# Optimization experiments

Hardware: AMD Instinct MI355X
Metric: run time of the kernel (lower is better)

The kernel has to match this reference:

```python
import jax, jax.numpy as jnp
import numpy as np

NEG_SLOPE = 0.2


def gat_layer(x, W, a_src, a_dst, b, src, dst, num_nodes, heads, out_c, concat):
    # Linear transform per head: [N, heads, out_c]
    h = (x @ W).reshape(num_nodes, heads, out_c)
    # Per-node attention logits for source/dest roles: [N, heads]
    e_src = jnp.einsum('nhc,hc->nh', h, a_src)
    e_dst = jnp.einsum('nhc,hc->nh', h, a_dst)
    # Edge-wise scores (gather), LeakyReLU: [E, heads]
    e = jax.nn.leaky_relu(e_src[src] + e_dst[dst], negative_slope=NEG_SLOPE)
    # Segment softmax over incoming edges of each destination node
    m = jax.ops.segment_max(e, dst, num_segments=num_nodes)
    ex = jnp.exp(e - m[dst])
    denom = jax.ops.segment_sum(ex, dst, num_segments=num_nodes)
    alpha = ex / denom[dst]                       # [E, heads]
    # Weighted scatter-aggregate of source messages: [N, heads, out_c]
    out = jax.ops.segment_sum(h[src] * alpha[:, :, None], dst, num_segments=num_nodes)
    if concat:
        out = out.reshape(num_nodes, heads * out_c)
    else:
        out = out.mean(axis=1)
    return out + b


def setup_inputs() -> dict:
    key = jax.random.key(0)
    ks = jax.random.split(key, 12)
    N, E = 50000, 800000
    in_c, out_c, heads = 128, 32, 4
    x = jax.random.normal(ks[0], (N, in_c), dtype=jnp.float32)
    edge_index = jax.random.randint(ks[1], (2, E), 0, N, dtype=jnp.int64)
    s1 = 1.0 / np.sqrt(in_c)
    W1 = jax.random.normal(ks[2], (in_c, heads * out_c), dtype=jnp.float32) * s1
    a_src1 = jax.random.normal(ks[3], (heads, out_c), dtype=jnp.float32) * 0.1
    a_dst1 = jax.random.normal(ks[4], (heads, out_c), dtype=jnp.float32) * 0.1
    b1 = jnp.zeros((heads * out_c,), dtype=jnp.float32)
    s2 = 1.0 / np.sqrt(heads * out_c)
    W2 = jax.random.normal(ks[5], (heads * out_c, out_c), dtype=jnp.float32) * s2
    a_src2 = jax.random.normal(ks[6], (1, out_c), dtype=jnp.float32) * 0.1
    a_dst2 = jax.random.normal(ks[7], (1, out_c), dtype=jnp.float32) * 0.1
    b2 = jnp.zeros((out_c,), dtype=jnp.float32)
    return {"x": x, "edge_index": edge_index, "W1": W1, "a_src1": a_src1,
            "a_dst1": a_dst1, "b1": b1, "W2": W2, "a_src2": a_src2,
            "a_dst2": a_dst2, "b2": b2}


def reference(x, edge_index, W1, a_src1, a_dst1, b1, W2, a_src2, a_dst2, b2):
    N = x.shape[0]
    heads, out_c = a_src1.shape
    # add_self_loops=True (PyG default)
    loops = jnp.arange(N, dtype=edge_index.dtype)
    src = jnp.concatenate([edge_index[0], loops])
    dst = jnp.concatenate([edge_index[1], loops])
    h1 = gat_layer(x, W1, a_src1, a_dst1, b1, src, dst, N, heads, out_c, concat=True)
    h1 = jax.nn.elu(h1)
    out = gat_layer(h1, W2, a_src2, a_dst2, b2, src, dst, N, 1, out_c, concat=False)
    return out
```

## Files before the change

kernel.cpp:

```cpp
#include <hip/hip_runtime.h>
#include <hip/hip_bf16.h>

#define LRELU_SLOPE 0.2f
#define NB_SHIFT 7

typedef __attribute__((ext_vector_type(8))) short short8;
typedef __attribute__((ext_vector_type(4))) float float4v;

__device__ inline float b2f(unsigned short u) {
    union { unsigned int i; float f; } v; v.i = ((unsigned int)u) << 16; return v.f;
}
__device__ inline unsigned short f2b(float f) {
    union { float f; unsigned int i; } v; v.f = f;
    unsigned int x = v.i;
    unsigned int r = x + 0x7fffu + ((x >> 16) & 1u);
    return (unsigned short)(r >> 16);
}
__device__ inline float lrelu(float x) { return x > 0.f ? x : LRELU_SLOPE * x; }

__global__ __launch_bounds__(256) void hist_kernel(const int* __restrict__ dst,
                                                   int E, int Etot, int nb, int nblk,
                                                   int chunk, int* __restrict__ cnt) {
    __shared__ int hist[512];
    int blk = blockIdx.x;
    for (int i = threadIdx.x; i < nb; i += 256) hist[i] = 0;
    __syncthreads();
    int lo = blk * chunk;
    int hi = lo + chunk; if (hi > Etot) hi = Etot;
    for (int i = lo + threadIdx.x; i < hi; i += 256) {
        int d = (i < E) ? dst[i] : (i - E);
        atomicAdd(&hist[d >> NB_SHIFT], 1);
    }
    __syncthreads();
    for (int b = threadIdx.x; b < nb; b += 256)
        cnt[b * nblk + blk] = hist[b];
}

__global__ __launch_bounds__(1024) void scanA_kernel(int* cnt, int* bsum, int M) {
    __shared__ int tile[1024];
    int i = blockIdx.x * 1024 + threadIdx.x;
    int v = (i < M) ? cnt[i] : 0;
    tile[threadIdx.x] = v;
    __syncthreads();
    for (int off = 1; off < 1024; off <<= 1) {
        int t = (threadIdx.x >= (unsigned)off) ? tile[threadIdx.x - off] : 0;
        __syncthreads();
        tile[threadIdx.x] += t;
        __syncthreads();
    }
    int incl = tile[threadIdx.x];
    if (i < M) cnt[i] = incl - v;
    if (threadIdx.x == 1023) bsum[blockIdx.x] = incl;
}

__global__ __launch_bounds__(256) void scanB_kernel(int* __restrict__ bsum, int nb) {
    __shared__ int tile[256];
    int v = (threadIdx.x < (unsigned)nb) ? bsum[threadIdx.x] : 0;
    tile[threadIdx.x] = v;
    __syncthreads();
    for (int off = 1; off < 256; off <<= 1) {
        int t = (threadIdx.x >= (unsigned)off) ? tile[threadIdx.x - off] : 0;
        __syncthreads();
        tile[threadIdx.x] += t;
        __syncthreads();
    }
    if (threadIdx.x < (unsigned)nb) bsum[threadIdx.x] = tile[threadIdx.x] - v;
}

__global__ __launch_bounds__(256) void partition_kernel(
        const int* __restrict__ src, const int* __restrict__ dst,
        int E, int Etot, int nb, int nblk, int chunk,
        const int* __restrict__ cnt, const int* __restrict__ boff,
        int2* __restrict__ bkt) {
    __shared__ int cur[512];
    int blk = blockIdx.x;
    for (int b = threadIdx.x; b < nb; b += 256) {
        int idx = b * nblk + blk;
        cur[b] = cnt[idx] + boff[idx >> 10];
    }
    __syncthreads();
    int lo = blk * chunk;
    int hi = lo + chunk; if (hi > Etot) hi = Etot;
    for (int i = lo + threadIdx.x; i < hi; i += 256) {
        int s, d;
        if (i < E) { s = src[i]; d = dst[i]; }
        else       { s = d = i - E; }
        int pos = atomicAdd(&cur[d >> NB_SHIFT], 1);
        bkt[pos] = make_int2(s, d);
    }
}

__global__ __launch_bounds__(256) void finalize_kernel(
        const int2* __restrict__ bkt, const int* __restrict__ cnt,
        const int* __restrict__ boff, int nb, int nblk,
        const float* __restrict__ es, const float* __restrict__ ed,
        int* __restrict__ ptr, int2* __restrict__ csr, float* __restrict__ w1,
        int N, int Etot) {
    __shared__ int deg[128];
    __shared__ int scn[128];
    __shared__ int cur[128];
    int b = blockIdx.x;
    int idx0 = b * nblk;
    int base = cnt[idx0] + boff[idx0 >> 10];
    int nextbase;
    if (b + 1 < nb) {
        int idx1 = (b + 1) * nblk;
        nextbase = cnt[idx1] + boff[idx1 >> 10];
    } else nextbase = Etot;
    int count = nextbase - base;
    int node0 = b << NB_SHIFT;
    int nodes = N - node0; if (nodes > 128) nodes = 128;

    if (threadIdx.x < 128) deg[threadIdx.x] = 0;
    __syncthreads();
    for (int i = threadIdx.x; i < count; i += 256)
        atomicAdd(&deg[bkt[base + i].y - node0], 1);
    __syncthreads();
    int v = (threadIdx.x < 128) ? deg[threadIdx.x] : 0;
    if (threadIdx.x < 128) scn[threadIdx.x] = v;
    __syncthreads();
    for (int off = 1; off < 128; off <<= 1) {
        int t = (threadIdx.x < 128 && threadIdx.x >= (unsigned)off) ? scn[threadIdx.x - off] : 0;
        __syncthreads();
        if (threadIdx.x < 128) scn[threadIdx.x] += t;
        __syncthreads();
    }
    if (threadIdx.x < 128) {
        int excl = scn[threadIdx.x] - v;
        cur[threadIdx.x] = excl;
        if (threadIdx.x < nodes) ptr[node0 + threadIdx.x] = base + excl;
    }
    if (b == nb - 1 && threadIdx.x == 0) ptr[N] = Etot;
    __syncthreads();
    for (int i = threadIdx.x; i < count; i += 256) {
        int2 sd = bkt[base + i];
        int pos = base + atomicAdd(&cur[sd.y - node0], 1);
        csr[pos] = sd;
        float4 a = *(const float4*)&es[sd.x * 4];
        float4 bb = *(const float4*)&ed[sd.y * 4];
        float4 ww;
        ww.x = __expf(lrelu(a.x + bb.x));
        ww.y = __expf(lrelu(a.y + bb.y));
        ww.z = __expf(lrelu(a.z + bb.z));
        ww.w = __expf(lrelu(a.w + bb.w));
        *(float4*)&w1[(size_t)pos * 4] = ww;
    }
}

__global__ __launch_bounds__(256) void gemm1_mfma_kernel(
        const float* __restrict__ x, const float* __restrict__ W1,
        unsigned short* __restrict__ h1b, int N) {
    __shared__ unsigned short xs[64][136];
    __shared__ unsigned short wt[128][136];
    int tid = threadIdx.x;
    int n0 = blockIdx.x * 64;

    for (int i = tid; i < 128 * 128; i += 256) {
        int k = i >> 7, n = i & 127;
        wt[n][k] = f2b(W1[i]);
    }
    for (int i = tid; i < 64 * 128; i += 256) {
        int r = i >> 7, k = i & 127;
        int row = n0 + r; if (row >= N) row = N - 1;
        xs[r][k] = f2b(x[(size_t)row * 128 + k]);
    }
    __syncthreads();

    int wave = tid >> 6;
    int lane = tid & 63;
    int lrow = lane & 15;
    int quad = lane >> 4;

    short8 afr[4];
#pragma unroll
    for (int kc = 0; kc < 4; kc++)
        afr[kc] = *(const short8*)&xs[wave * 16 + lrow][kc * 32 + quad * 8];

#pragma unroll
    for (int ct = 0; ct < 8; ct++) {
        float4v acc = {0.f, 0.f, 0.f, 0.f};
#pragma unroll
        for (int kc = 0; kc < 4; kc++) {
            short8 bfr = *(const short8*)&wt[ct * 16 + lrow][kc * 32 + quad * 8];
            acc = __builtin_amdgcn_mfma_f32_16x16x32_bf16(afr[kc], bfr, acc, 0, 0, 0);
        }
#pragma unroll
        for (int r = 0; r < 4; r++) {
            int grow = n0 + wave * 16 + quad * 4 + r;
            if (grow < N)
                h1b[grow * 128 + ct * 16 + lrow] = f2b(acc[r]);
        }
    }
}

__global__ __launch_bounds__(256) void gemm2_mfma_kernel(
        const unsigned short* __restrict__ h1e, const float* __restrict__ W2,
        unsigned short* __restrict__ h2b, int N) {
    __shared__ unsigned short xs[64][136];
    __shared__ unsigned short wt[32][136];
    int tid = threadIdx.x;
    int n0 = blockIdx.x * 64;

    for (int i = tid; i < 128 * 32; i += 256) {
        int k = i >> 5, n = i & 31;
        wt[n][k] = f2b(W2[i]);
    }
    {
        const unsigned int* srcp = (const unsigned int*)(h1e + (size_t)n0 * 128);
        int rows = (N - n0) < 64 ? (N - n0) : 64;
        int maxu = rows * 64;
        for (int i = tid; i < 4096; i += 256) {
            unsigned int v = (i < maxu) ? srcp[i] : 0u;
            int r = i >> 6, cp = (i & 63) << 1;
            *(unsigned int*)&xs[r][cp] = v;
        }
    }
    __syncthreads();

    int wave = tid >> 6;
    int lane = tid & 63;
    int lrow = lane & 15;
    int quad = lane >> 4;

    short8 afr[4];
#pragma unroll
    for (int kc = 0; kc < 4; kc++)
        afr[kc] = *(const short8*)&xs[wave * 16 + lrow][kc * 32 + quad * 8];

#pragma unroll
    for (int ct = 0; ct < 2; ct++) {
        float4v acc = {0.f, 0.f, 0.f, 0.f};
#pragma unroll
        for (int kc = 0; kc < 4; kc++) {
            short8 bfr = *(const short8*)&wt[ct * 16 + lrow][kc * 32 + quad * 8];
            acc = __builtin_amdgcn_mfma_f32_16x16x32_bf16(afr[kc], bfr, acc, 0, 0, 0);
        }
#pragma unroll
        for (int r = 0; r < 4; r++) {
            int grow = n0 + wave * 16 + quad * 4 + r;
            if (grow < N)
                h2b[(size_t)grow * 32 + ct * 16 + lrow] = f2b(acc[r]);
        }
    }
}

__global__ void dots1_kernel(const unsigned short* __restrict__ h1b,
                             const float* __restrict__ a_src,
                             const float* __restrict__ a_dst,
                             float* __restrict__ es, float* __restrict__ ed,
                             int N4) {
    int t = blockIdx.x * 256 + threadIdx.x;
    if (t >= N4) return;
    int h = t & 3;
    const unsigned int* hp = (const unsigned int*)(h1b + (size_t)t * 32);
    const float* ap = a_src + h * 32;
    const float* bp = a_dst + h * 32;
    float s = 0.f, d = 0.f;
#pragma unroll
    for (int j = 0; j < 16; j++) {
        unsigned int u = hp[j];
        float v0 = b2f((unsigned short)(u & 0xffffu));
        float v1 = b2f((unsigned short)(u >> 16));
        s += v0 * ap[2 * j] + v1 * ap[2 * j + 1];
        d += v0 * bp[2 * j] + v1 * bp[2 * j + 1];
    }
    es[t] = s; ed[t] = d;
}

__global__ void dots2_kernel(const unsigned short* __restrict__ h2b,
                             const float* __restrict__ a_src,
                             const float* __restrict__ a_dst,
                             float* __restrict__ es, float* __restrict__ ed,
                             int N) {
    int t = blockIdx.x * 256 + threadIdx.x;
    if (t >= N) return;
    const unsigned int* hp = (const unsigned int*)(h2b + (size_t)t * 32);
    const float* ap = a_src;
    const float* bp = a_dst;
    float s = 0.f, d = 0.f;
#pragma unroll
    for (int j = 0; j < 16; j++) {
        unsigned int u = hp[j];
        float v0 = b2f((unsigned short)(u & 0xffffu));
        float v1 = b2f((unsigned short)(u >> 16));
        s += v0 * ap[2 * j] + v1 * ap[2 * j + 1];
        d += v0 * bp[2 * j] + v1 * bp[2 * j + 1];
    }
    es[t] = s; ed[t] = d;
}

__global__ void weights2_kernel(const int2* __restrict__ csr,
                                const float* __restrict__ es,
                                const float* __restrict__ ed,
                                float* __restrict__ w2, int Etot) {
    int e = blockIdx.x * 256 + threadIdx.x;
    if (e >= Etot) return;
    int2 sd = csr[e];
    w2[e] = __expf(lrelu(es[sd.x] + ed[sd.y]));
}

__global__ __launch_bounds__(256) void agg1_kernel(
        const unsigned int* __restrict__ h1u, const float* __restrict__ w1,
        const int2* __restrict__ csr, const int* __restrict__ ptr,
        const float* __restrict__ b1, unsigned int* __restrict__ h1e_u, int N) {
    int wave = threadIdx.x >> 6;
    int lane = threadIdx.x & 63;
    int n = blockIdx.x * 4 + wave;
    if (n >= N) return;
    int h = lane >> 4;
    int start = ptr[n], end = ptr[n + 1];
    float acc0 = 0.f, acc1 = 0.f, wsum = 0.f;
    int i = start;
    for (; i + 4 <= end; i += 4) {
        int s0 = csr[i + 0].x;
        int s1 = csr[i + 1].x;
        int s2 = csr[i + 2].x;
        int s3 = csr[i + 3].x;
        float v0 = w1[(size_t)(i + 0) * 4 + h];
        float v1 = w1[(size_t)(i + 1) * 4 + h];
        float v2 = w1[(size_t)(i + 2) * 4 + h];
        float v3 = w1[(size_t)(i + 3) * 4 + h];
        unsigned int g0 = h1u[(s0 << 6) + lane];
        unsigned int g1 = h1u[(s1 << 6) + lane];
        unsigned int g2 = h1u[(s2 << 6) + lane];
        unsigned int g3 = h1u[(s3 << 6) + lane];
        acc0 += v0 * b2f((unsigned short)(g0 & 0xffffu))
              + v1 * b2f((unsigned short)(g1 & 0xffffu))
              + v2 * b2f((unsigned short)(g2 & 0xffffu))
              + v3 * b2f((unsigned short)(g3 & 0xffffu));
        acc1 += v0 * b2f((unsigned short)(g0 >> 16))
              + v1 * b2f((unsigned short)(g1 >> 16))
              + v2 * b2f((unsigned short)(g2 >> 16))
              + v3 * b2f((unsigned short)(g3 >> 16));
        wsum += (v0 + v1) + (v2 + v3);
    }
    for (; i < end; i++) {
        int s = csr[i].x;
        float v = w1[(size_t)i * 4 + h];
        unsigned int g = h1u[(s << 6) + lane];
        acc0 += v * b2f((unsigned short)(g & 0xffffu));
        acc1 += v * b2f((unsigned short)(g >> 16));
        wsum += v;
    }
    float r = 1.f / wsum;
    float2 bb = ((const float2*)b1)[lane];
    float o0 = acc0 * r + bb.x;
    float o1 = acc1 * r + bb.y;
    o0 = o0 > 0.f ? o0 : __expf(o0) - 1.f;
    o1 = o1 > 0.f ? o1 : __expf(o1) - 1.f;
    h1e_u[(n << 6) + lane] = (unsigned int)f2b(o0) | ((unsigned int)f2b(o1) << 16);
}

__global__ __launch_bounds__(256) void agg2_kernel(
        const unsigned int* __restrict__ h2u, const float* __restrict__ w2,
        const int2* __restrict__ csr, const int* __restrict__ ptr,
        const float* __restrict__ b2, float* __restrict__ out, int N) {
    int lane = threadIdx.x & 63;
    int g = lane >> 4;
    int n = blockIdx.x * 16 + (threadIdx.x >> 6) * 4 + g;
    if (n >= N) return;
    int cl = lane & 15;
    int start = ptr[n], end = ptr[n + 1];
    float acc0 = 0.f, acc1 = 0.f, wsum = 0.f;
    int i = start;
    for (; i + 4 <= end; i += 4) {
        int s0 = csr[i + 0].x;
        int s1 = csr[i + 1].x;
        int s2 = csr[i + 2].x;
        int s3 = csr[i + 3].x;
        float v0 = w2[i + 0];
        float v1 = w2[i + 1];
        float v2 = w2[i + 2];
        float v3 = w2[i + 3];
        unsigned int g0 = h2u[(s0 << 4) + cl];
        unsigned int g1 = h2u[(s1 << 4) + cl];
        unsigned int g2 = h2u[(s2 << 4) + cl];
        unsigned int g3 = h2u[(s3 << 4) + cl];
        acc0 += v0 * b2f((unsigned short)(g0 & 0xffffu))
              + v1 * b2f((unsigned short)(g1 & 0xffffu))
              + v2 * b2f((unsigned short)(g2 & 0xffffu))
              + v3 * b2f((unsigned short)(g3 & 0xffffu));
        acc1 += v0 * b2f((unsigned short)(g0 >> 16))
              + v1 * b2f((unsigned short)(g1 >> 16))
              + v2 * b2f((unsigned short)(g2 >> 16))
              + v3 * b2f((unsigned short)(g3 >> 16));
        wsum += (v0 + v1) + (v2 + v3);
    }
    for (; i < end; i++) {
        int s = csr[i].x;
        float v = w2[i];
        unsigned int gg = h2u[(s << 4) + cl];
        acc0 += v * b2f((unsigned short)(gg & 0xffffu));
        acc1 += v * b2f((unsigned short)(gg >> 16));
        wsum += v;
    }
    float r = 1.f / wsum;
    float2 bb = ((const float2*)b2)[cl];
    float2 o;
    o.x = acc0 * r + bb.x;
    o.y = acc1 * r + bb.y;
    ((float2*)out)[(size_t)n * 16 + cl] = o;
}

extern "C" void kernel_launch(void* const* d_in, const int* in_sizes, int n_in,
                              void* d_out, int out_size, void* d_ws, size_t ws_size,
                              hipStream_t stream) {
    const float* x      = (const float*)d_in[0];
    const int*   ei     = (const int*)  d_in[1];
    const float* W1     = (const float*)d_in[2];
    const float* a_src1 = (const float*)d_in[3];
    const float* a_dst1 = (const float*)d_in[4];
    const float* b1     = (const float*)d_in[5];
    const float* W2     = (const float*)d_in[6];
    const float* a_src2 = (const float*)d_in[7];
    const float* a_dst2 = (const float*)d_in[8];
    const float* b2     = (const float*)d_in[9];
    float* outp = (float*)d_out;

    const int N = in_sizes[0] / 128;
    const int E = in_sizes[1] / 2;
    const int Etot = E + N;

    const int* src = ei;
    const int* dst = ei + E;

    const int nb   = (N + 127) >> 7;
    const int nblk = 128;
    const int chunk = (Etot + nblk - 1) / nblk;
    const int M = nb * nblk;
    const int nbA = (M + 1023) / 1024;

    char* w = (char*)d_ws;
    unsigned short* h1b = (unsigned short*)(w + 0);
    unsigned short* h1e = (unsigned short*)(w + 12800000);
    unsigned short* h2b = (unsigned short*)(w + 25600000);
    float* es1  = (float*)(w + 28800000);
    float* ed1  = (float*)(w + 29600000);
    float* es2  = (float*)(w + 30400000);
    float* ed2  = (float*)(w + 30600000);
    int*   ptr  = (int*)  (w + 30800000);
    int*   bsum = (int*)  (w + 31000064);
    int*   cnt  = (int*)  (w + 31001088);
    int2*  csr  = (int2*) (w + 31201280);
    int2*  bkt  = (int2*) (w + 38001280);
    float* w1   = (float*)(w + 44801280);
    float* w2   = (float*)(w + 58401280);

    gemm1_mfma_kernel<<<(N + 63) / 64, 256, 0, stream>>>(x, W1, h1b, N);
    dots1_kernel<<<(N * 4 + 255) / 256, 256, 0, stream>>>(h1b, a_src1, a_dst1, es1, ed1, N * 4);

    hist_kernel<<<nblk, 256, 0, stream>>>(dst, E, Etot, nb, nblk, chunk, cnt);
    scanA_kernel<<<nbA, 1024, 0, stream>>>(cnt, bsum, M);
    scanB_kernel<<<1, 256, 0, stream>>>(bsum, nbA);
    partition_kernel<<<nblk, 256, 0, stream>>>(src, dst, E, Etot, nb, nblk, chunk,
                                               cnt, bsum, bkt);
    finalize_kernel<<<nb, 256, 0, stream>>>(bkt, cnt, bsum, nb, nblk, es1, ed1,
                                            ptr, csr, w1, N, Etot);

    agg1_kernel<<<(N + 3) / 4, 256, 0, stream>>>((const unsigned int*)h1b, w1, csr, ptr,
                                                 b1, (unsigned int*)h1e, N);

    gemm2_mfma_kernel<<<(N + 63) / 64, 256, 0, stream>>>(h1e, W2, h2b, N);
    dots2_kernel<<<(N + 255) / 256, 256, 0, stream>>>(h2b, a_src2, a_dst2, es2, ed2, N);
    weights2_kernel<<<(Etot + 255) / 256, 256, 0, stream>>>(csr, es2, ed2, w2, Etot);
    agg2_kernel<<<(N + 15) / 16, 256, 0, stream>>>((const unsigned int*)h2b, w2, csr, ptr,
                                                   b2, outp, N);
}
```

Baseline: 229.8 us.

## Fuse attention dots into GEMMs, compute layer-2 weights inline, shrink CSR

The per-node attention dot products move into the epilogues of both MFMA GEMM kernels, which stage the bf16 output tile in shared memory; this removes the dots1 and dots2 launches and their reread of h. The layer-2 edge weights are now computed on the fly inside agg2, which drops the weights2 kernel and the w2 buffer. The CSR now stores only source indices (int instead of int2), cutting its write and read traffic. agg1 is unrolled to 8 edges per step to keep more gathers in flight. In exchange, agg2 recomputes exp per edge and the GEMMs gain extra barriers and epilogue work.

```diff
diff --git a/kernel.cpp b/kernel.cpp
--- a/kernel.cpp
+++ b/kernel.cpp
@@ -94,7 +94,7 @@
         const int2* __restrict__ bkt, const int* __restrict__ cnt,
         const int* __restrict__ boff, int nb, int nblk,
         const float* __restrict__ es, const float* __restrict__ ed,
-        int* __restrict__ ptr, int2* __restrict__ csr, float* __restrict__ w1,
+        int* __restrict__ ptr, int* __restrict__ csr_src, float* __restrict__ w1,
         int N, int Etot) {
     __shared__ int deg[128];
     __shared__ int scn[128];
@@ -135,7 +135,7 @@
     for (int i = threadIdx.x; i < count; i += 256) {
         int2 sd = bkt[base + i];
         int pos = base + atomicAdd(&cur[sd.y - node0], 1);
-        csr[pos] = sd;
+        csr_src[pos] = sd.x;
         float4 a = *(const float4*)&es[sd.x * 4];
         float4 bb = *(const float4*)&ed[sd.y * 4];
         float4 ww;
@@ -149,7 +149,9 @@
 
 __global__ __launch_bounds__(256) void gemm1_mfma_kernel(
         const float* __restrict__ x, const float* __restrict__ W1,
-        unsigned short* __restrict__ h1b, int N) {
+        const float* __restrict__ a_src, const float* __restrict__ a_dst,
+        unsigned short* __restrict__ h1b, float* __restrict__ es,
+        float* __restrict__ ed, int N) {
     __shared__ unsigned short xs[64][136];
     __shared__ unsigned short wt[128][136];
     int tid = threadIdx.x;
@@ -175,6 +177,7 @@
 #pragma unroll
     for (int kc = 0; kc < 4; kc++)
         afr[kc] = *(const short8*)&xs[wave * 16 + lrow][kc * 32 + quad * 8];
+    __syncthreads();
 
 #pragma unroll
     for (int ct = 0; ct < 8; ct++) {
@@ -186,16 +189,42 @@
         }
 #pragma unroll
         for (int r = 0; r < 4; r++) {
-            int grow = n0 + wave * 16 + quad * 4 + r;
+            int lr = wave * 16 + quad * 4 + r;
+            int grow = n0 + lr;
+            unsigned short hb = f2b(acc[r]);
+            xs[lr][ct * 16 + lrow] = hb;
             if (grow < N)
-                h1b[grow * 128 + ct * 16 + lrow] = f2b(acc[r]);
-        }
+                h1b[grow * 128 + ct * 16 + lrow] = hb;
+        }
+    }
+    __syncthreads();
+
+    int row = tid >> 2, h = tid & 3;
+    int rg = n0 + row;
+    if (rg < N) {
+        const float* ap = a_src + h * 32;
+        const float* bp = a_dst + h * 32;
+        float s = 0.f, d = 0.f;
+#pragma unroll
+        for (int c2 = 0; c2 < 16; c2++) {
+            unsigned int u = *(const unsigned int*)&xs[row][h * 32 + 2 * c2];
+            float v0 = b2f((unsigned short)(u & 0xffffu));
+            float v1 = b2f((unsigned short)(u >> 16));
+            float2 a = *(const float2*)&ap[2 * c2];
+            float2 b = *(const float2*)&bp[2 * c2];
+            s += v0 * a.x + v1 * a.y;
+            d += v0 * b.x + v1 * b.y;
+        }
+        es[rg * 4 + h] = s;
+        ed[rg * 4 + h] = d;
     }
 }
 
 __global__ __launch_bounds__(256) void gemm2_mfma_kernel(
         const unsigned short* __restrict__ h1e, const float* __restrict__ W2,
-        unsigned short* __restrict__ h2b, int N) {
+        const float* __restrict__ a_src, const float* __restrict__ a_dst,
+        unsigned short* __restrict__ h2b, float* __restrict__ es,
+        float* __restrict__ ed, int N) {
     __shared__ unsigned short xs[64][136];
     __shared__ unsigned short wt[32][136];
     int tid = threadIdx.x;
@@ -226,6 +255,7 @@
 #pragma unroll
     for (int kc = 0; kc < 4; kc++)
         afr[kc] = *(const short8*)&xs[wave * 16 + lrow][kc * 32 + quad * 8];
+    __syncthreads();
 
 #pragma unroll
     for (int ct = 0; ct < 2; ct++) {
@@ -237,71 +267,39 @@
         }
 #pragma unroll
         for (int r = 0; r < 4; r++) {
-            int grow = n0 + wave * 16 + quad * 4 + r;
+            int lr = wave * 16 + quad * 4 + r;
+            int grow = n0 + lr;
+            unsigned short hb = f2b(acc[r]);
+            xs[lr][ct * 16 + lrow] = hb;
             if (grow < N)
-                h2b[(size_t)grow * 32 + ct * 16 + lrow] = f2b(acc[r]);
-        }
-    }
-}
-
-__global__ void dots1_kernel(const unsigned short* __restrict__ h1b,
-                             const float* __restrict__ a_src,
-                             const float* __restrict__ a_dst,
-                             float* __restrict__ es, float* __restrict__ ed,
-                             int N4) {
-    int t = blockIdx.x * 256 + threadIdx.x;
-    if (t >= N4) return;
-    int h = t & 3;
-    const unsigned int* hp = (const unsigned int*)(h1b + (size_t)t * 32);
-    const float* ap = a_src + h * 32;
-    const float* bp = a_dst + h * 32;
-    float s = 0.f, d = 0.f;
-#pragma unroll
-    for (int j = 0; j < 16; j++) {
-        unsigned int u = hp[j];
-        float v0 = b2f((unsigned short)(u & 0xffffu));
-        float v1 = b2f((unsigned short)(u >> 16));
-        s += v0 * ap[2 * j] + v1 * ap[2 * j + 1];
-        d += v0 * bp[2 * j] + v1 * bp[2 * j + 1];
-    }
-    es[t] = s; ed[t] = d;
-}
-
-__global__ void dots2_kernel(const unsigned short* __restrict__ h2b,
-                             const float* __restrict__ a_src,
-                             const float* __restrict__ a_dst,
-                             float* __restrict__ es, float* __restrict__ ed,
-                             int N) {
-    int t = blockIdx.x * 256 + threadIdx.x;
-    if (t >= N) return;
-    const unsigned int* hp = (const unsigned int*)(h2b + (size_t)t * 32);
-    const float* ap = a_src;
-    const float* bp = a_dst;
-    float s = 0.f, d = 0.f;
-#pragma unroll
-    for (int j = 0; j < 16; j++) {
-        unsigned int u = hp[j];
-        float v0 = b2f((unsigned short)(u & 0xffffu));
-        float v1 = b2f((unsigned short)(u >> 16));
-        s += v0 * ap[2 * j] + v1 * ap[2 * j + 1];
-        d += v0 * bp[2 * j] + v1 * bp[2 * j + 1];
-    }
-    es[t] = s; ed[t] = d;
-}
-
-__global__ void weights2_kernel(const int2* __restrict__ csr,
-                                const float* __restrict__ es,
-                                const float* __restrict__ ed,
-                                float* __restrict__ w2, int Etot) {
-    int e = blockIdx.x * 256 + threadIdx.x;
-    if (e >= Etot) return;
-    int2 sd = csr[e];
-    w2[e] = __expf(lrelu(es[sd.x] + ed[sd.y]));
+                h2b[(size_t)grow * 32 + ct * 16 + lrow] = hb;
+        }
+    }
+    __syncthreads();
+
+    if (tid < 64) {
+        int rg = n0 + tid;
+        if (rg < N) {
+            float s = 0.f, d = 0.f;
+#pragma unroll
+            for (int c2 = 0; c2 < 16; c2++) {
+                unsigned int u = *(const unsigned int*)&xs[tid][2 * c2];
+                float v0 = b2f((unsigned short)(u & 0xffffu));
+                float v1 = b2f((unsigned short)(u >> 16));
+                float2 a = *(const float2*)&a_src[2 * c2];
+                float2 b = *(const float2*)&a_dst[2 * c2];
+                s += v0 * a.x + v1 * a.y;
+                d += v0 * b.x + v1 * b.y;
+            }
+            es[rg] = s;
+            ed[rg] = d;
+        }
+    }
 }
 
 __global__ __launch_bounds__(256) void agg1_kernel(
         const unsigned int* __restrict__ h1u, const float* __restrict__ w1,
-        const int2* __restrict__ csr, const int* __restrict__ ptr,
+        const int* __restrict__ csr, const int* __restrict__ ptr,
         const float* __restrict__ b1, unsigned int* __restrict__ h1e_u, int N) {
     int wave = threadIdx.x >> 6;
     int lane = threadIdx.x & 63;
@@ -311,31 +309,38 @@
     int start = ptr[n], end = ptr[n + 1];
     float acc0 = 0.f, acc1 = 0.f, wsum = 0.f;
     int i = start;
+    for (; i + 8 <= end; i += 8) {
+        int s[8]; float v[8]; unsigned int g[8];
+#pragma unroll
+        for (int k = 0; k < 8; k++) s[k] = csr[i + k];
+#pragma unroll
+        for (int k = 0; k < 8; k++) v[k] = w1[(size_t)(i + k) * 4 + h];
+#pragma unroll
+        for (int k = 0; k < 8; k++) g[k] = h1u[(s[k] << 6) + lane];
+#pragma unroll
+        for (int k = 0; k < 8; k++) {
+            acc0 += v[k] * b2f((unsigned short)(g[k] & 0xffffu));
+            acc1 += v[k] * b2f((unsigned short)(g[k] >> 16));
+            wsum += v[k];
+        }
+    }
     for (; i + 4 <= end; i += 4) {
-        int s0 = csr[i + 0].x;
-        int s1 = csr[i + 1].x;
-        int s2 = csr[i + 2].x;
-        int s3 = csr[i + 3].x;
-        float v0 = w1[(size_t)(i + 0) * 4 + h];
-        float v1 = w1[(size_t)(i + 1) * 4 + h];
-        float v2 = w1[(size_t)(i + 2) * 4 + h];
-        float v3 = w1[(size_t)(i + 3) * 4 + h];
-        unsigned int g0 = h1u[(s0 << 6) + lane];
-        unsigned int g1 = h1u[(s1 << 6) + lane];
-        unsigned int g2 = h1u[(s2 << 6) + lane];
-        unsigned int g3 = h1u[(s3 << 6) + lane];
-        acc0 += v0 * b2f((unsigned short)(g0 & 0xffffu))
-              + v1 * b2f((unsigned short)(g1 & 0xffffu))
-              + v2 * b2f((unsigned short)(g2 & 0xffffu))
-              + v3 * b2f((unsigned short)(g3 & 0xffffu));
-        acc1 += v0 * b2f((unsigned short)(g0 >> 16))
-              + v1 * b2f((unsigned short)(g1 >> 16))
-              + v2 * b2f((unsigned short)(g2 >> 16))
-              + v3 * b2f((unsigned short)(g3 >> 16));
-        wsum += (v0 + v1) + (v2 + v3);
+        int s[4]; float v[4]; unsigned int g[4];
+#pragma unroll
+        for (int k = 0; k < 4; k++) s[k] = csr[i + k];
+#pragma unroll
+        for (int k = 0; k < 4; k++) v[k] = w1[(size_t)(i + k) * 4 + h];
+#pragma unroll
+        for (int k = 0; k < 4; k++) g[k] = h1u[(s[k] << 6) + lane];
+#pragma unroll
+        for (int k = 0; k < 4; k++) {
+            acc0 += v[k] * b2f((unsigned short)(g[k] & 0xffffu));
+            acc1 += v[k] * b2f((unsigned short)(g[k] >> 16));
+            wsum += v[k];
+        }
     }
     for (; i < end; i++) {
-        int s = csr[i].x;
+        int s = csr[i];
         float v = w1[(size_t)i * 4 + h];
         unsigned int g = h1u[(s << 6) + lane];
         acc0 += v * b2f((unsigned short)(g & 0xffffu));
@@ -352,46 +357,40 @@
 }
 
 __global__ __launch_bounds__(256) void agg2_kernel(
-        const unsigned int* __restrict__ h2u, const float* __restrict__ w2,
-        const int2* __restrict__ csr, const int* __restrict__ ptr,
-        const float* __restrict__ b2, float* __restrict__ out, int N) {
+        const unsigned int* __restrict__ h2u, const float* __restrict__ es,
+        const float* __restrict__ ed, const int* __restrict__ csr,
+        const int* __restrict__ ptr, const float* __restrict__ b2,
+        float* __restrict__ out, int N) {
     int lane = threadIdx.x & 63;
-    int g = lane >> 4;
-    int n = blockIdx.x * 16 + (threadIdx.x >> 6) * 4 + g;
+    int n = blockIdx.x * 16 + (threadIdx.x >> 6) * 4 + (lane >> 4);
     if (n >= N) return;
     int cl = lane & 15;
+    float edl = ed[n];
     int start = ptr[n], end = ptr[n + 1];
     float acc0 = 0.f, acc1 = 0.f, wsum = 0.f;
     int i = start;
     for (; i + 4 <= end; i += 4) {
-        int s0 = csr[i + 0].x;
-        int s1 = csr[i + 1].x;
-        int s2 = csr[i + 2].x;
-        int s3 = csr[i + 3].x;
-        float v0 = w2[i + 0];
-        float v1 = w2[i + 1];
-        float v2 = w2[i + 2];
-        float v3 = w2[i + 3];
-        unsigned int g0 = h2u[(s0 << 4) + cl];
-        unsigned int g1 = h2u[(s1 << 4) + cl];
-        unsigned int g2 = h2u[(s2 << 4) + cl];
-        unsigned int g3 = h2u[(s3 << 4) + cl];
-        acc0 += v0 * b2f((unsigned short)(g0 & 0xffffu))
-              + v1 * b2f((unsigned short)(g1 & 0xffffu))
-              + v2 * b2f((unsigned short)(g2 & 0xffffu))
-              + v3 * b2f((unsigned short)(g3 & 0xffffu));
-        acc1 += v0 * b2f((unsigned short)(g0 >> 16))
-              + v1 * b2f((unsigned short)(g1 >> 16))
-              + v2 * b2f((unsigned short)(g2 >> 16))
-              + v3 * b2f((unsigned short)(g3 >> 16));
-        wsum += (v0 + v1) + (v2 + v3);
+        int s[4]; float e[4]; unsigned int g[4];
+#pragma unroll
+        for (int k = 0; k < 4; k++) s[k] = csr[i + k];
+#pragma unroll
+        for (int k = 0; k < 4; k++) e[k] = es[s[k]];
+#pragma unroll
+        for (int k = 0; k < 4; k++) g[k] = h2u[(s[k] << 4) + cl];
+#pragma unroll
+        for (int k = 0; k < 4; k++) {
+            float v = __expf(lrelu(e[k] + edl));
+            acc0 += v * b2f((unsigned short)(g[k] & 0xffffu));
+            acc1 += v * b2f((unsigned short)(g[k] >> 16));
+            wsum += v;
+        }
     }
     for (; i < end; i++) {
-        int s = csr[i].x;
-        float v = w2[i];
-        unsigned int gg = h2u[(s << 4) + cl];
-        acc0 += v * b2f((unsigned short)(gg & 0xffffu));
-        acc1 += v * b2f((unsigned short)(gg >> 16));
+        int s = csr[i];
+        float v = __expf(lrelu(es[s] + edl));
+        unsigned int g = h2u[(s << 4) + cl];
+        acc0 += v * b2f((unsigned short)(g & 0xffffu));
+        acc1 += v * b2f((unsigned short)(g >> 16));
         wsum += v;
     }
     float r = 1.f / wsum;
@@ -441,13 +440,12 @@
     int*   ptr  = (int*)  (w + 30800000);
     int*   bsum = (int*)  (w + 31000064);
     int*   cnt  = (int*)  (w + 31001088);
-    int2*  csr  = (int2*) (w + 31201280);
-    int2*  bkt  = (int2*) (w + 38001280);
-    float* w1   = (float*)(w + 44801280);
-    float* w2   = (float*)(w + 58401280);
-
-    gemm1_mfma_kernel<<<(N + 63) / 64, 256, 0, stream>>>(x, W1, h1b, N);
-    dots1_kernel<<<(N * 4 + 255) / 256, 256, 0, stream>>>(h1b, a_src1, a_dst1, es1, ed1, N * 4);
+    int*   csr_src = (int*)(w + 31201280);
+    int2*  bkt  = (int2*) (w + 34601280);
+    float* w1   = (float*)(w + 41401280);
+
+    gemm1_mfma_kernel<<<(N + 63) / 64, 256, 0, stream>>>(x, W1, a_src1, a_dst1,
+                                                         h1b, es1, ed1, N);
 
     hist_kernel<<<nblk, 256, 0, stream>>>(dst, E, Etot, nb, nblk, chunk, cnt);
     scanA_kernel<<<nbA, 1024, 0, stream>>>(cnt, bsum, M);
@@ -455,14 +453,14 @@
     partition_kernel<<<nblk, 256, 0, stream>>>(src, dst, E, Etot, nb, nblk, chunk,
                                                cnt, bsum, bkt);
     finalize_kernel<<<nb, 256, 0, stream>>>(bkt, cnt, bsum, nb, nblk, es1, ed1,
-                                            ptr, csr, w1, N, Etot);
-
-    agg1_kernel<<<(N + 3) / 4, 256, 0, stream>>>((const unsigned int*)h1b, w1, csr, ptr,
-                                                 b1, (unsigned int*)h1e, N);
-
-    gemm2_mfma_kernel<<<(N + 63) / 64, 256, 0, stream>>>(h1e, W2, h2b, N);
-    dots2_kernel<<<(N + 255) / 256, 256, 0, stream>>>(h2b, a_src2, a_dst2, es2, ed2, N);
-    weights2_kernel<<<(Etot + 255) / 256, 256, 0, stream>>>(csr, es2, ed2, w2, Etot);
-    agg2_kernel<<<(N + 15) / 16, 256, 0, stream>>>((const unsigned int*)h2b, w2, csr, ptr,
-                                                   b2, outp, N);
-}
+                                            ptr, csr_src, w1, N, Etot);
+
+    agg1_kernel<<<(N + 3) / 4, 256, 0, stream>>>((const unsigned int*)h1b, w1,
+                                                 csr_src, ptr, b1,
+                                                 (unsigned int*)h1e, N);
+
+    gemm2_mfma_kernel<<<(N + 63) / 64, 256, 0, stream>>>(h1e, W2, a_src2, a_dst2,
+                                                         h2b, es2, ed2, N);
+    agg2_kernel<<<(N + 15) / 16, 256, 0, stream>>>((const unsigned int*)h2b, es2, ed2,
+                                                   csr_src, ptr, b2, outp, N);
+}
```

Result: faster. 217.3 us (-5.4%).
